# Optimization experiments

Hardware: AMD Instinct MI355X
Metric: run time of the kernel (lower is better)

The kernel has to match this reference:

```python
import jax, jax.numpy as jnp
import numpy as np

C = 512

def _xavier(key, shape, gain=1.0):
    fan_in, fan_out = shape[1], shape[0]
    a = gain * np.sqrt(6.0 / (fan_in + fan_out))
    return jax.random.uniform(key, shape, jnp.float32, -a, a)

def setup_inputs() -> dict:
    key = jax.random.key(0)
    ks = jax.random.split(key, 5)
    x = jax.random.normal(ks[0], (32, C, 32, 32), jnp.float32)
    # 1x1 conv weights as [out_ch, in_ch]; biases zero-init per module
    Wq = _xavier(ks[1], (C, C))
    Wk = _xavier(ks[2], (C, C))
    Wv = _xavier(ks[3], (C, C))
    Wo = _xavier(ks[4], (C, C), gain=1e-05)
    zeros = jnp.zeros((C,), jnp.float32)
    return {"x": x, "Wq": Wq, "bq": zeros, "Wk": Wk, "bk": zeros,
            "Wv": Wv, "bv": zeros, "Wo": Wo, "bo": zeros}

def _proj(x, W, b):
    # 1x1 conv: x [B,C,H,W], W [Cout,Cin] -> [B,Cout,H,W]
    return jnp.einsum('bchw,oc->bohw', x, W) + b[None, :, None, None]

def reference(x, Wq, bq, Wk, bk, Wv, bv, Wo, bo):
    B, Cc, H, W = x.shape
    q = _proj(x, Wq, bq).transpose(0, 2, 3, 1).reshape(B, H * W, Cc)  # [B,HW,C]
    k = _proj(x, Wk, bk).reshape(B, Cc, H * W)                        # [B,C,HW]
    v = _proj(x, Wv, bv).transpose(0, 2, 3, 1).reshape(B, H * W, Cc)  # [B,HW,C]
    w = jnp.einsum('bnc,bcm->bnm', q, k) * (Cc ** -0.5)               # [B,HW,HW]
    w = jax.nn.softmax(w, axis=-1)
    h = jnp.einsum('bnm,bmc->bnc', w, v)                              # [B,HW,C]
    h = h.reshape(B, H, W, Cc).transpose(0, 3, 1, 2)                  # [B,C,H,W]
    h = _proj(h, Wo, bo)
    return x + h
```

## Files before the change

### kernel.cpp

```cpp
#include <hip/hip_runtime.h>
#include <stdint.h>


#define CD 512
#define NSP 1024
#define SCALE_EXP2 0.06376339f

using bf16x8 = __attribute__((ext_vector_type(8))) short;
using f32x4  = __attribute__((ext_vector_type(4))) float;
typedef long i64v;

__device__ __forceinline__ unsigned short f2bf(float f) {
    union { float f; unsigned int i; } v; v.f = f;
    unsigned int r = v.i + 0x7FFFu + ((v.i >> 16) & 1u);
    return (unsigned short)(r >> 16);
}
__device__ __forceinline__ unsigned char f2f8(float f) {
    unsigned int r;
    asm("v_cvt_pk_fp8_f32 %0, %1, %1" : "=v"(r) : "v"(f));
    return (unsigned char)(r & 0xffu);
}
__device__ __forceinline__ unsigned int f4_to_f8x4(float a, float b, float c, float d) {
    unsigned int r = 0;
    asm("v_cvt_pk_fp8_f32 %0, %2, %3\n\t"
        "v_cvt_pk_fp8_f32 %0, %4, %5 op_sel:[0,0,1]"
        : "=v"(r) : "0"(r), "v"(a), "v"(b), "v"(c), "v"(d));
    return r;
}
__device__ __forceinline__ void gl_lds16(const void* g, void* l) {
    __builtin_amdgcn_global_load_lds(
        (const __attribute__((address_space(1))) void*)g,
        (__attribute__((address_space(3))) void*)l, 16, 0, 0);
}

__global__ __launch_bounds__(256) void cvt_all(
    const float* __restrict__ Wq, const float* __restrict__ Wk,
    const float* __restrict__ Wv, const float* __restrict__ Wo,
    const float* __restrict__ bq, const float* __restrict__ bk,
    unsigned char* __restrict__ w8, unsigned short* __restrict__ wob,
    float* __restrict__ bqk)
{
    int idx = blockIdx.x * 256 + threadIdx.x;
    int which = idx >> 18, off = idx & 262143;
    if (which < 3) {
        const float* src = which == 0 ? Wq : which == 1 ? Wk : Wv;
        w8[idx] = f2f8(src[off]);
    } else {
        wob[off] = f2bf(Wo[off]);
    }
    if (idx < 1024) bqk[idx] = (idx < 512) ? bq[idx] : bk[idx - 512];
}

__global__ __launch_bounds__(256) void transpose_x(const float* __restrict__ x,
                                                   unsigned char* __restrict__ xt) {
    __shared__ float t[32][33];
    int b = blockIdx.z;
    int n0 = blockIdx.x * 32, c0 = blockIdx.y * 32;
    const float* xb = x + (size_t)b * CD * NSP;
    unsigned char* xtb = xt + (size_t)b * NSP * CD;
    int tx = threadIdx.x, ty = threadIdx.y;
    #pragma unroll
    for (int i = 0; i < 4; ++i)
        t[ty + i * 8][tx] = xb[(size_t)(c0 + ty + i * 8) * NSP + n0 + tx];
    __syncthreads();
    #pragma unroll
    for (int i = 0; i < 4; ++i)
        xtb[(size_t)(n0 + ty + i * 8) * CD + c0 + tx] = f2f8(t[tx][ty + i * 8]);
}

template<int BIAS_MODE>
__global__ __launch_bounds__(256)
void gemm_bt8(const unsigned char* __restrict__ A,
              const unsigned char* __restrict__ B,
              unsigned char* __restrict__ C8,
              const float* __restrict__ bias,
              int K, int lda, int ldb, int ldc,
              long sA, long sB, long sC)
{
    __shared__ __align__(16) unsigned char As[2][128 * 64];
    __shared__ __align__(16) unsigned char Bs[2][128 * 64];

    const int z = blockIdx.z;
    const unsigned char* Ab = A + (size_t)z * sA + (size_t)blockIdx.y * 128 * lda;
    const unsigned char* Bb = B + (size_t)z * sB + (size_t)blockIdx.x * 128 * ldb;

    const int t = threadIdx.x;
    const int lane = t & 63;
    const int wave = t >> 6;
    const int wr = wave >> 1, wc = wave & 1;
    const int lr = lane & 15, lk = lane >> 4;

    f32x4 acc[4][4] = {};

    const int KT = K >> 6;
    auto stage = [&](int kt, int buf) {
        int k0 = kt << 6;
        #pragma unroll
        for (int i = 0; i < 2; ++i) {
            int rb = i * 64 + wave * 16;
            int row = rb + (lane >> 2);
            int src = (lane & 3) ^ ((row >> 1) & 3);
            gl_lds16(Ab + (size_t)row * lda + k0 + src * 16, &As[buf][rb * 64]);
            gl_lds16(Bb + (size_t)row * ldb + k0 + src * 16, &Bs[buf][rb * 64]);
        }
    };
    stage(0, 0);
    for (int kt = 0; kt < KT; ++kt) {
        int cur = kt & 1;
        if (kt + 1 < KT) {
            stage(kt + 1, cur ^ 1);
            asm volatile("s_waitcnt vmcnt(4)" ::: "memory");
        } else {
            asm volatile("s_waitcnt vmcnt(0)" ::: "memory");
        }
        __builtin_amdgcn_s_barrier();
        const unsigned char* Ac = &As[cur][0];
        const unsigned char* Bc = &Bs[cur][0];
        #pragma unroll
        for (int kk = 0; kk < 2; ++kk) {
            int c16 = kk * 2 + (lk >> 1);
            int half = (lk & 1) * 8;
            i64v af[4], bfr[4];
            #pragma unroll
            for (int f = 0; f < 4; ++f) {
                int arow = wr * 64 + f * 16 + lr;
                af[f] = *(const i64v*)&Ac[arow * 64 + ((c16 ^ ((arow >> 1) & 3)) << 4) + half];
                int brow = wc * 64 + f * 16 + lr;
                bfr[f] = *(const i64v*)&Bc[brow * 64 + ((c16 ^ ((brow >> 1) & 3)) << 4) + half];
            }
            #pragma unroll
            for (int fm = 0; fm < 4; ++fm)
                #pragma unroll
                for (int fn = 0; fn < 4; ++fn)
                    acc[fm][fn] = __builtin_amdgcn_mfma_f32_16x16x32_fp8_fp8(
                        af[fm], bfr[fn], acc[fm][fn], 0, 0, 0);
        }
        asm volatile("s_waitcnt lgkmcnt(0)" ::: "memory");
        __builtin_amdgcn_s_barrier();
    }

    const int m0 = blockIdx.y * 128;
    const int n0 = blockIdx.x * 128;
    unsigned char* Cp = C8 + (size_t)z * sC;
    #pragma unroll
    for (int fm = 0; fm < 4; ++fm) {
        #pragma unroll
        for (int fn = 0; fn < 4; ++fn) {
            int col = n0 + wc * 64 + fn * 16 + lr;
            int rowb = m0 + wr * 64 + fm * 16 + lk * 4;
            #pragma unroll
            for (int j = 0; j < 4; ++j) {
                int row = rowb + j;
                float v = acc[fm][fn][j];
                if (BIAS_MODE == 1) v += bias[col];
                if (BIAS_MODE == 2) v += bias[row];
                Cp[(size_t)row * ldc + col] = f2f8(v);
            }
        }
    }
}

__global__ __launch_bounds__(256)
void gemm_bt_out(const unsigned short* __restrict__ A,
                 const unsigned short* __restrict__ B,
                 float* __restrict__ Cf,
                 const float* __restrict__ bias,
                 const float* __restrict__ resid,
                 int K, int lda, int ldb, int ldc,
                 long sB, long sC, long sR)
{
    __shared__ __align__(16) unsigned short As[2][128 * 64];
    __shared__ __align__(16) unsigned short Bs[2][128 * 64];

    const int z = blockIdx.z;
    const unsigned short* Ab = A + (size_t)blockIdx.y * 128 * lda;
    const unsigned short* Bb = B + (size_t)z * sB + (size_t)blockIdx.x * 128 * ldb;

    const int t = threadIdx.x;
    const int lane = t & 63;
    const int wave = t >> 6;
    const int wr = wave >> 1, wc = wave & 1;
    const int lr = lane & 15, lk = lane >> 4;

    f32x4 acc[4][4] = {};

    const int KT = K >> 6;
    auto stage = [&](int kt, int buf) {
        int k0 = kt << 6;
        #pragma unroll
        for (int i = 0; i < 4; ++i) {
            int rb = i * 32 + wave * 8;
            int row = rb + (lane >> 3);
            int ch = (lane & 7) ^ (row & 7);
            gl_lds16(Ab + (size_t)row * lda + k0 + ch * 8, &As[buf][rb * 64]);
            gl_lds16(Bb + (size_t)row * ldb + k0 + ch * 8, &Bs[buf][rb * 64]);
        }
    };
    stage(0, 0);
    for (int kt = 0; kt < KT; ++kt) {
        int cur = kt & 1;
        if (kt + 1 < KT) {
            stage(kt + 1, cur ^ 1);
            asm volatile("s_waitcnt vmcnt(8)" ::: "memory");
        } else {
            asm volatile("s_waitcnt vmcnt(0)" ::: "memory");
        }
        __builtin_amdgcn_s_barrier();
        const unsigned short* Ac = &As[cur][0];
        const unsigned short* Bc = &Bs[cur][0];
        #pragma unroll
        for (int kk = 0; kk < 2; ++kk) {
            bf16x8 af[4], bfr[4];
            #pragma unroll
            for (int f = 0; f < 4; ++f) {
                int arow = wr * 64 + f * 16 + lr;
                af[f] = *(const bf16x8*)&Ac[(arow << 6) + ((((kk << 2) | lk) ^ (arow & 7)) << 3)];
                int brow = wc * 64 + f * 16 + lr;
                bfr[f] = *(const bf16x8*)&Bc[(brow << 6) + ((((kk << 2) | lk) ^ (brow & 7)) << 3)];
            }
            #pragma unroll
            for (int fm = 0; fm < 4; ++fm)
                #pragma unroll
                for (int fn = 0; fn < 4; ++fn)
                    acc[fm][fn] = __builtin_amdgcn_mfma_f32_16x16x32_bf16(
                        af[fm], bfr[fn], acc[fm][fn], 0, 0, 0);
        }
        asm volatile("s_waitcnt lgkmcnt(0)" ::: "memory");
        __builtin_amdgcn_s_barrier();
    }

    const int m0 = blockIdx.y * 128;
    const int n0 = blockIdx.x * 128;
    float* Co = Cf + (size_t)z * sC;
    const float* rp = resid + (size_t)z * sR;
    #pragma unroll
    for (int fm = 0; fm < 4; ++fm) {
        #pragma unroll
        for (int fn = 0; fn < 4; ++fn) {
            int col = n0 + wc * 64 + fn * 16 + lr;
            int rowb = m0 + wr * 64 + fm * 16 + lk * 4;
            #pragma unroll
            for (int j = 0; j < 4; ++j) {
                int row = rowb + j;
                float v = acc[fm][fn][j] + bias[row] + rp[(size_t)row * ldc + col];
                Co[(size_t)row * ldc + col] = v;
            }
        }
    }
}

__global__ __launch_bounds__(512, 2)
void flash_attn(const unsigned char* __restrict__ Q,
                const unsigned char* __restrict__ Kg,
                const unsigned char* __restrict__ Vg,
                unsigned short* __restrict__ H)
{
    __shared__ __align__(16) unsigned char Ks[2][64 * 512];
    __shared__ __align__(16) unsigned char Vs[2][512 * 64];
    __shared__ __align__(16) unsigned char Ps[128 * 72];
    __shared__ float Ls[128];
    __shared__ int flag;

    const int p = blockIdx.x;
    const int b  = ((p >> 6) << 3) + (p & 7);
    const int qt = (p >> 3) & 7;

    const int tid = threadIdx.x;
    const int w = tid >> 6, lane = tid & 63;
    const int lr = lane & 15, lk = lane >> 4;
    const int q0 = qt * 128 + w * 16;

    i64v qf[16];
    const unsigned char* qp = Q + ((size_t)b * NSP + q0 + lr) * 1024 + lk * 8;
    #pragma unroll
    for (int st = 0; st < 16; ++st) qf[st] = *(const i64v*)(qp + st * 32);

    f32x4 o[8][4] = {};
    float m = -3.0e38f, l = 0.f;

    const unsigned char* Kb = Kg + (size_t)b * NSP * 1024;
    const unsigned char* Vb = Vg + (size_t)b * CD * 1024;

    auto stageK = [&](int t, int buf) {
        int kv0 = t * 64;
        #pragma unroll
        for (int i = 0; i < 4; ++i) {
            int rb = i * 16 + w * 2;
            int row = rb + (lane >> 5);
            int src = (lane & 31) ^ (row & 7);
            gl_lds16(Kb + (size_t)(kv0 + row) * 1024 + src * 16, &Ks[buf][rb * 512]);
        }
    };
    auto stageV = [&](int t, int buf) {
        int kv0 = t * 64;
        #pragma unroll
        for (int i = 0; i < 4; ++i) {
            int cb = i * 128 + w * 16;
            int c = cb + (lane >> 2);
            int src = (lane & 3) ^ ((c >> 1) & 3);
            gl_lds16(Vb + (size_t)c * 1024 + kv0 + src * 16, &Vs[buf][cb * 64]);
        }
    };

    if (tid == 0) flag = -1;
    stageK(0, 0); stageV(0, 0);
    asm volatile("s_waitcnt vmcnt(0) lgkmcnt(0)" ::: "memory");
    __builtin_amdgcn_s_barrier();

    for (int t = 0; t < 16; ++t) {
        const int cur = t & 1;
        if (t < 15) { stageK(t + 1, cur ^ 1); stageV(t + 1, cur ^ 1); }

        f32x4 s[4] = {};
        const unsigned char* Kc = &Ks[cur][0];
        __builtin_amdgcn_s_setprio(1);
        #pragma unroll
        for (int st = 0; st < 16; ++st) {
            int c16 = st * 2 + (lk >> 1);
            int half = (lk & 1) * 8;
            #pragma unroll
            for (int kvf = 0; kvf < 4; ++kvf) {
                int row = kvf * 16 + lr;
                i64v kf = *(const i64v*)&Kc[row * 512 + ((c16 ^ (row & 7)) << 4) + half];
                s[kvf] = __builtin_amdgcn_mfma_f32_16x16x32_fp8_fp8(kf, qf[st], s[kvf], 0, 0, 0);
            }
        }
        __builtin_amdgcn_s_setprio(0);

        #pragma unroll
        for (int kvf = 0; kvf < 4; ++kvf)
            #pragma unroll
            for (int j = 0; j < 4; ++j) s[kvf][j] *= SCALE_EXP2;

        float pm = fmaxf(fmaxf(fmaxf(s[0][0], s[0][1]), fmaxf(s[0][2], s[0][3])),
                         fmaxf(fmaxf(s[1][0], s[1][1]), fmaxf(s[1][2], s[1][3])));
        pm = fmaxf(pm, fmaxf(fmaxf(fmaxf(s[2][0], s[2][1]), fmaxf(s[2][2], s[2][3])),
                             fmaxf(fmaxf(s[3][0], s[3][1]), fmaxf(s[3][2], s[3][3]))));
        pm = fmaxf(pm, __shfl_xor(pm, 16));
        pm = fmaxf(pm, __shfl_xor(pm, 32));
        bool ev = !__all(pm - m <= 8.0f);
        float mn = fmaxf(m, pm);
        float sc = ev ? exp2f(m - mn) : 1.0f;
        if (ev) { m = mn; l *= sc; }
        if (lk == 0) Ls[w * 16 + lr] = sc;
        if (ev && lane == 0) flag = t;

        float rs = 0.f;
        #pragma unroll
        for (int kvf = 0; kvf < 4; ++kvf)
            #pragma unroll
            for (int j = 0; j < 4; ++j) {
                s[kvf][j] = exp2f(s[kvf][j] - m);
                rs += s[kvf][j];
            }
        rs += __shfl_xor(rs, 16);
        rs += __shfl_xor(rs, 32);
        l += rs;

        #pragma unroll
        for (int kvf = 0; kvf < 4; ++kvf) {
            unsigned int pk = f4_to_f8x4(s[kvf][0], s[kvf][1], s[kvf][2], s[kvf][3]);
            *(unsigned int*)&Ps[(w * 16 + lr) * 72 + kvf * 16 + lk * 4] = pk;
        }
        asm volatile("s_waitcnt lgkmcnt(0)" ::: "memory");
        __builtin_amdgcn_s_barrier();

        if (flag == t) {
            #pragma unroll
            for (int qf2 = 0; qf2 < 8; ++qf2) {
                f32x4 scv = *(const f32x4*)&Ls[qf2 * 16 + lk * 4];
                #pragma unroll
                for (int cf = 0; cf < 4; ++cf) {
                    o[qf2][cf][0] *= scv[0]; o[qf2][cf][1] *= scv[1];
                    o[qf2][cf][2] *= scv[2]; o[qf2][cf][3] *= scv[3];
                }
            }
        }
        const unsigned char* Vc2 = &Vs[cur][0];
        __builtin_amdgcn_s_setprio(1);
        #pragma unroll
        for (int ks = 0; ks < 2; ++ks) {
            int c16 = ks * 2 + (lk >> 1);
            int half = (lk & 1) * 8;
            i64v vfr[4];
            #pragma unroll
            for (int cf = 0; cf < 4; ++cf) {
                int c = w * 64 + cf * 16 + lr;
                vfr[cf] = *(const i64v*)&Vc2[c * 64 + ((c16 ^ ((c >> 1) & 3)) << 4) + half];
            }
            #pragma unroll
            for (int qf2 = 0; qf2 < 8; ++qf2) {
                i64v pa = *(const i64v*)&Ps[(qf2 * 16 + lr) * 72 + ks * 32 + lk * 8];
                #pragma unroll
                for (int cf = 0; cf < 4; ++cf)
                    o[qf2][cf] = __builtin_amdgcn_mfma_f32_16x16x32_fp8_fp8(
                        pa, vfr[cf], o[qf2][cf], 0, 0, 0);
            }
        }
        __builtin_amdgcn_s_setprio(0);
        asm volatile("s_waitcnt vmcnt(0) lgkmcnt(0)" ::: "memory");
        __builtin_amdgcn_s_barrier();
    }

    if (lk == 0) Ls[w * 16 + lr] = 1.0f / l;
    asm volatile("s_waitcnt lgkmcnt(0)" ::: "memory");
    __builtin_amdgcn_s_barrier();
    unsigned short* Hp = H + ((size_t)b * NSP + qt * 128) * CD + w * 64;
    #pragma unroll
    for (int qf2 = 0; qf2 < 8; ++qf2) {
        f32x4 li = *(const f32x4*)&Ls[qf2 * 16 + lk * 4];
        #pragma unroll
        for (int cf = 0; cf < 4; ++cf) {
            #pragma unroll
            for (int j = 0; j < 4; ++j)
                Hp[(size_t)(qf2 * 16 + lk * 4 + j) * CD + cf * 16 + lr] = f2bf(o[qf2][cf][j] * li[j]);
        }
    }
}

extern "C" void kernel_launch(void* const* d_in, const int* in_sizes, int n_in,
                              void* d_out, int out_size, void* d_ws, size_t ws_size,
                              hipStream_t stream)
{
    const float* x  = (const float*)d_in[0];
    const float* Wq = (const float*)d_in[1];
    const float* bq = (const float*)d_in[2];
    const float* Wk = (const float*)d_in[3];
    const float* bk = (const float*)d_in[4];
    const float* Wv = (const float*)d_in[5];
    const float* bv = (const float*)d_in[6];
    const float* Wo = (const float*)d_in[7];
    const float* bo = (const float*)d_in[8];
    float* out = (float*)d_out;

    unsigned char* w = (unsigned char*)d_ws;
    unsigned char*  W8  = w;
    unsigned short* Wob = (unsigned short*)(w + 786432);
    float*          bqk = (float*)(w + 1310720);
    unsigned char*  Xt8 = w + 1314816;
    unsigned char*  QK8 = w + 18092032;
    unsigned char*  Vc8 = w + 51646464;
    unsigned short* Hb  = (unsigned short*)(w + 68423680);

    cvt_all<<<4096, 256, 0, stream>>>(Wq, Wk, Wv, Wo, bq, bk, W8, Wob, bqk);
    transpose_x<<<dim3(32, 16, 32), dim3(32, 8), 0, stream>>>(x, Xt8);

    gemm_bt8<1><<<dim3(8, 256, 1), 256, 0, stream>>>(
        Xt8, W8, QK8, bqk, 512, 512, 512, 1024, 0, 0, 0);

    gemm_bt8<2><<<dim3(8, 4, 32), 256, 0, stream>>>(
        W8 + 524288, Xt8, Vc8, bv, 512, 512, 512, 1024, 0, 524288, 524288);

    flash_attn<<<256, 512, 0, stream>>>(QK8, QK8 + 512, Vc8, Hb);

    gemm_bt_out<<<dim3(8, 4, 32), 256, 0, stream>>>(
        Wob, Hb, out, bo, x, 512, 512, 512, 1024, 524288, 524288, 524288);
}
```

Measured before the change: 205.0 us.

## Warp-specialize flash attention into QK-softmax and PV/loader wave groups

Splits the flash-attention block into 4 waves that compute QK scores and softmax (each handling 32 query rows) and 8 waves that stage K/V tiles and accumulate P·V. P, the rescale factors and the flags are double-buffered in LDS so that QK for tile t+1 overlaps PV for tile t, and staging runs two tiles ahead. The intent is to hide softmax and load latency behind the matrix units. In exchange the block grows to 768 threads with a tighter per-thread register budget, and correctness now depends on barrier counts matching exactly between the two wave groups.

```diff
diff --git a/kernel.cpp b/kernel.cpp
--- a/kernel.cpp
+++ b/kernel.cpp
@@ -249,7 +249,7 @@
     }
 }
 
-__global__ __launch_bounds__(512, 2)
+__global__ __launch_bounds__(768, 3)
 void flash_attn(const unsigned char* __restrict__ Q,
                 const unsigned char* __restrict__ Kg,
                 const unsigned char* __restrict__ Vg,
@@ -257,9 +257,10 @@
 {
     __shared__ __align__(16) unsigned char Ks[2][64 * 512];
     __shared__ __align__(16) unsigned char Vs[2][512 * 64];
-    __shared__ __align__(16) unsigned char Ps[128 * 72];
-    __shared__ float Ls[128];
-    __shared__ int flag;
+    __shared__ __align__(16) unsigned char Ps[2][128 * 72];
+    __shared__ __align__(16) float Ls[2][128];
+    __shared__ __align__(16) float Lfin[128];
+    __shared__ int flags[2];
 
     const int p = blockIdx.x;
     const int b  = ((p >> 6) << 3) + (p & 7);
@@ -268,152 +269,185 @@
     const int tid = threadIdx.x;
     const int w = tid >> 6, lane = tid & 63;
     const int lr = lane & 15, lk = lane >> 4;
-    const int q0 = qt * 128 + w * 16;
-
-    i64v qf[16];
-    const unsigned char* qp = Q + ((size_t)b * NSP + q0 + lr) * 1024 + lk * 8;
-    #pragma unroll
-    for (int st = 0; st < 16; ++st) qf[st] = *(const i64v*)(qp + st * 32);
-
-    f32x4 o[8][4] = {};
-    float m = -3.0e38f, l = 0.f;
+
+    if (tid == 0) { flags[0] = -1; flags[1] = -1; }
 
     const unsigned char* Kb = Kg + (size_t)b * NSP * 1024;
     const unsigned char* Vb = Vg + (size_t)b * CD * 1024;
 
-    auto stageK = [&](int t, int buf) {
-        int kv0 = t * 64;
-        #pragma unroll
-        for (int i = 0; i < 4; ++i) {
-            int rb = i * 16 + w * 2;
-            int row = rb + (lane >> 5);
-            int src = (lane & 31) ^ (row & 7);
-            gl_lds16(Kb + (size_t)(kv0 + row) * 1024 + src * 16, &Ks[buf][rb * 512]);
-        }
-    };
-    auto stageV = [&](int t, int buf) {
-        int kv0 = t * 64;
-        #pragma unroll
-        for (int i = 0; i < 4; ++i) {
-            int cb = i * 128 + w * 16;
-            int c = cb + (lane >> 2);
-            int src = (lane & 3) ^ ((c >> 1) & 3);
-            gl_lds16(Vb + (size_t)c * 1024 + kv0 + src * 16, &Vs[buf][cb * 64]);
-        }
-    };
-
-    if (tid == 0) flag = -1;
-    stageK(0, 0); stageV(0, 0);
-    asm volatile("s_waitcnt vmcnt(0) lgkmcnt(0)" ::: "memory");
-    __builtin_amdgcn_s_barrier();
-
-    for (int t = 0; t < 16; ++t) {
-        const int cur = t & 1;
-        if (t < 15) { stageK(t + 1, cur ^ 1); stageV(t + 1, cur ^ 1); }
-
-        f32x4 s[4] = {};
-        const unsigned char* Kc = &Ks[cur][0];
-        __builtin_amdgcn_s_setprio(1);
+    if (w < 4) {
+        const int q0 = qt * 128 + w * 32;
+        i64v qf0[16], qf1[16];
+        const unsigned char* qp = Q + ((size_t)b * NSP + q0 + lr) * 1024 + lk * 8;
         #pragma unroll
         for (int st = 0; st < 16; ++st) {
-            int c16 = st * 2 + (lk >> 1);
-            int half = (lk & 1) * 8;
+            qf0[st] = *(const i64v*)(qp + st * 32);
+            qf1[st] = *(const i64v*)(qp + 16 * 1024 + st * 32);
+        }
+        float m0 = -3.0e38f, m1 = -3.0e38f, l0 = 0.f, l1 = 0.f;
+
+        auto qksm = [&](int tau) {
+            const int pb = tau & 1;
+            const unsigned char* Kc = &Ks[pb][0];
+            f32x4 s0[4] = {}, s1[4] = {};
+            __builtin_amdgcn_s_setprio(1);
+            #pragma unroll
+            for (int st = 0; st < 16; ++st) {
+                int c16 = st * 2 + (lk >> 1);
+                int half = (lk & 1) * 8;
+                #pragma unroll
+                for (int kvf = 0; kvf < 4; ++kvf) {
+                    int row = kvf * 16 + lr;
+                    i64v kf = *(const i64v*)&Kc[row * 512 + ((c16 ^ (row & 7)) << 4) + half];
+                    s0[kvf] = __builtin_amdgcn_mfma_f32_16x16x32_fp8_fp8(kf, qf0[st], s0[kvf], 0, 0, 0);
+                    s1[kvf] = __builtin_amdgcn_mfma_f32_16x16x32_fp8_fp8(kf, qf1[st], s1[kvf], 0, 0, 0);
+                }
+            }
+            __builtin_amdgcn_s_setprio(0);
+            #pragma unroll
+            for (int kvf = 0; kvf < 4; ++kvf)
+                #pragma unroll
+                for (int j = 0; j < 4; ++j) {
+                    s0[kvf][j] *= SCALE_EXP2;
+                    s1[kvf][j] *= SCALE_EXP2;
+                }
+            float pm0 = fmaxf(fmaxf(fmaxf(s0[0][0], s0[0][1]), fmaxf(s0[0][2], s0[0][3])),
+                              fmaxf(fmaxf(s0[1][0], s0[1][1]), fmaxf(s0[1][2], s0[1][3])));
+            pm0 = fmaxf(pm0, fmaxf(fmaxf(fmaxf(s0[2][0], s0[2][1]), fmaxf(s0[2][2], s0[2][3])),
+                                   fmaxf(fmaxf(s0[3][0], s0[3][1]), fmaxf(s0[3][2], s0[3][3]))));
+            float pm1 = fmaxf(fmaxf(fmaxf(s1[0][0], s1[0][1]), fmaxf(s1[0][2], s1[0][3])),
+                              fmaxf(fmaxf(s1[1][0], s1[1][1]), fmaxf(s1[1][2], s1[1][3])));
+            pm1 = fmaxf(pm1, fmaxf(fmaxf(fmaxf(s1[2][0], s1[2][1]), fmaxf(s1[2][2], s1[2][3])),
+                                   fmaxf(fmaxf(s1[3][0], s1[3][1]), fmaxf(s1[3][2], s1[3][3]))));
+            pm0 = fmaxf(pm0, __shfl_xor(pm0, 16));
+            pm0 = fmaxf(pm0, __shfl_xor(pm0, 32));
+            pm1 = fmaxf(pm1, __shfl_xor(pm1, 16));
+            pm1 = fmaxf(pm1, __shfl_xor(pm1, 32));
+            bool ev = !__all(fmaxf(pm0 - m0, pm1 - m1) <= 8.0f);
+            float sc0 = 1.f, sc1 = 1.f;
+            if (ev) {
+                float n0 = fmaxf(m0, pm0); sc0 = exp2f(m0 - n0); m0 = n0; l0 *= sc0;
+                float n1 = fmaxf(m1, pm1); sc1 = exp2f(m1 - n1); m1 = n1; l1 *= sc1;
+            }
+            if (lk == 0) { Ls[pb][w * 32 + lr] = sc0; Ls[pb][w * 32 + 16 + lr] = sc1; }
+            if (ev && lane == 0) flags[pb] = tau;
+            float rs0 = 0.f, rs1 = 0.f;
             #pragma unroll
             for (int kvf = 0; kvf < 4; ++kvf) {
-                int row = kvf * 16 + lr;
-                i64v kf = *(const i64v*)&Kc[row * 512 + ((c16 ^ (row & 7)) << 4) + half];
-                s[kvf] = __builtin_amdgcn_mfma_f32_16x16x32_fp8_fp8(kf, qf[st], s[kvf], 0, 0, 0);
-            }
-        }
-        __builtin_amdgcn_s_setprio(0);
-
-        #pragma unroll
-        for (int kvf = 0; kvf < 4; ++kvf)
-            #pragma unroll
-            for (int j = 0; j < 4; ++j) s[kvf][j] *= SCALE_EXP2;
-
-        float pm = fmaxf(fmaxf(fmaxf(s[0][0], s[0][1]), fmaxf(s[0][2], s[0][3])),
-                         fmaxf(fmaxf(s[1][0], s[1][1]), fmaxf(s[1][2], s[1][3])));
-        pm = fmaxf(pm, fmaxf(fmaxf(fmaxf(s[2][0], s[2][1]), fmaxf(s[2][2], s[2][3])),
-                             fmaxf(fmaxf(s[3][0], s[3][1]), fmaxf(s[3][2], s[3][3]))));
-        pm = fmaxf(pm, __shfl_xor(pm, 16));
-        pm = fmaxf(pm, __shfl_xor(pm, 32));
-        bool ev = !__all(pm - m <= 8.0f);
-        float mn = fmaxf(m, pm);
-        float sc = ev ? exp2f(m - mn) : 1.0f;
-        if (ev) { m = mn; l *= sc; }
-        if (lk == 0) Ls[w * 16 + lr] = sc;
-        if (ev && lane == 0) flag = t;
-
-        float rs = 0.f;
-        #pragma unroll
-        for (int kvf = 0; kvf < 4; ++kvf)
-            #pragma unroll
-            for (int j = 0; j < 4; ++j) {
-                s[kvf][j] = exp2f(s[kvf][j] - m);
-                rs += s[kvf][j];
-            }
-        rs += __shfl_xor(rs, 16);
-        rs += __shfl_xor(rs, 32);
-        l += rs;
-
-        #pragma unroll
-        for (int kvf = 0; kvf < 4; ++kvf) {
-            unsigned int pk = f4_to_f8x4(s[kvf][0], s[kvf][1], s[kvf][2], s[kvf][3]);
-            *(unsigned int*)&Ps[(w * 16 + lr) * 72 + kvf * 16 + lk * 4] = pk;
-        }
+                #pragma unroll
+                for (int j = 0; j < 4; ++j) {
+                    s0[kvf][j] = exp2f(s0[kvf][j] - m0); rs0 += s0[kvf][j];
+                    s1[kvf][j] = exp2f(s1[kvf][j] - m1); rs1 += s1[kvf][j];
+                }
+                unsigned int pk0 = f4_to_f8x4(s0[kvf][0], s0[kvf][1], s0[kvf][2], s0[kvf][3]);
+                unsigned int pk1 = f4_to_f8x4(s1[kvf][0], s1[kvf][1], s1[kvf][2], s1[kvf][3]);
+                *(unsigned int*)&Ps[pb][(w * 32 + lr) * 72 + kvf * 16 + lk * 4] = pk0;
+                *(unsigned int*)&Ps[pb][(w * 32 + 16 + lr) * 72 + kvf * 16 + lk * 4] = pk1;
+            }
+            rs0 += __shfl_xor(rs0, 16); rs0 += __shfl_xor(rs0, 32); l0 += rs0;
+            rs1 += __shfl_xor(rs1, 16); rs1 += __shfl_xor(rs1, 32); l1 += rs1;
+        };
+
+        __builtin_amdgcn_s_barrier();
+        qksm(0);
         asm volatile("s_waitcnt lgkmcnt(0)" ::: "memory");
         __builtin_amdgcn_s_barrier();
-
-        if (flag == t) {
-            #pragma unroll
-            for (int qf2 = 0; qf2 < 8; ++qf2) {
-                f32x4 scv = *(const f32x4*)&Ls[qf2 * 16 + lk * 4];
+        for (int t = 0; t < 16; ++t) {
+            if (t < 15) qksm(t + 1);
+            asm volatile("s_waitcnt lgkmcnt(0)" ::: "memory");
+            __builtin_amdgcn_s_barrier();
+        }
+        if (lk == 0) { Lfin[w * 32 + lr] = 1.f / l0; Lfin[w * 32 + 16 + lr] = 1.f / l1; }
+        asm volatile("s_waitcnt lgkmcnt(0)" ::: "memory");
+        __builtin_amdgcn_s_barrier();
+    } else {
+        const int wp = w - 4;
+        auto stageK = [&](int t, int buf) {
+            int kv0 = t * 64;
+            #pragma unroll
+            for (int i = 0; i < 4; ++i) {
+                int rb = i * 16 + wp * 2;
+                int row = rb + (lane >> 5);
+                int src = (lane & 31) ^ (row & 7);
+                gl_lds16(Kb + (size_t)(kv0 + row) * 1024 + src * 16, &Ks[buf][rb * 512]);
+            }
+        };
+        auto stageV = [&](int t, int buf) {
+            int kv0 = t * 64;
+            #pragma unroll
+            for (int i = 0; i < 4; ++i) {
+                int cb = wp * 64 + i * 16;
+                int c = cb + (lane >> 2);
+                int src = (lane & 3) ^ ((c >> 1) & 3);
+                gl_lds16(Vb + (size_t)c * 1024 + kv0 + src * 16, &Vs[buf][cb * 64]);
+            }
+        };
+        f32x4 o[8][4] = {};
+
+        stageK(0, 0); stageV(0, 0);
+        asm volatile("s_waitcnt vmcnt(0)" ::: "memory");
+        __builtin_amdgcn_s_barrier();
+        stageK(1, 1); stageV(1, 1);
+        asm volatile("s_waitcnt vmcnt(0)" ::: "memory");
+        __builtin_amdgcn_s_barrier();
+
+        for (int t = 0; t < 16; ++t) {
+            const int pb = t & 1;
+            if (t < 14) stageK(t + 2, pb);
+            if (flags[pb] == t) {
+                #pragma unroll
+                for (int qf2 = 0; qf2 < 8; ++qf2) {
+                    f32x4 scv = *(const f32x4*)&Ls[pb][qf2 * 16 + lk * 4];
+                    #pragma unroll
+                    for (int cf = 0; cf < 4; ++cf) {
+                        o[qf2][cf][0] *= scv[0]; o[qf2][cf][1] *= scv[1];
+                        o[qf2][cf][2] *= scv[2]; o[qf2][cf][3] *= scv[3];
+                    }
+                }
+            }
+            const unsigned char* Vc = &Vs[pb][0];
+            __builtin_amdgcn_s_setprio(1);
+            #pragma unroll
+            for (int ks = 0; ks < 2; ++ks) {
+                int c16 = ks * 2 + (lk >> 1);
+                int half = (lk & 1) * 8;
+                i64v vfr[4];
                 #pragma unroll
                 for (int cf = 0; cf < 4; ++cf) {
-                    o[qf2][cf][0] *= scv[0]; o[qf2][cf][1] *= scv[1];
-                    o[qf2][cf][2] *= scv[2]; o[qf2][cf][3] *= scv[3];
-                }
-            }
-        }
-        const unsigned char* Vc2 = &Vs[cur][0];
-        __builtin_amdgcn_s_setprio(1);
-        #pragma unroll
-        for (int ks = 0; ks < 2; ++ks) {
-            int c16 = ks * 2 + (lk >> 1);
-            int half = (lk & 1) * 8;
-            i64v vfr[4];
+                    int c = wp * 64 + cf * 16 + lr;
+                    vfr[cf] = *(const i64v*)&Vc[c * 64 + ((c16 ^ ((c >> 1) & 3)) << 4) + half];
+                }
+                #pragma unroll
+                for (int qf2 = 0; qf2 < 8; ++qf2) {
+                    i64v pa = *(const i64v*)&Ps[pb][(qf2 * 16 + lr) * 72 + ks * 32 + lk * 8];
+                    #pragma unroll
+                    for (int cf = 0; cf < 4; ++cf)
+                        o[qf2][cf] = __builtin_amdgcn_mfma_f32_16x16x32_fp8_fp8(
+                            pa, vfr[cf], o[qf2][cf], 0, 0, 0);
+                }
+            }
+            __builtin_amdgcn_s_setprio(0);
+            asm volatile("s_waitcnt lgkmcnt(0)" ::: "memory");
+            if (t < 14) {
+                stageV(t + 2, pb);
+                asm volatile("s_waitcnt vmcnt(4)" ::: "memory");
+            } else {
+                asm volatile("s_waitcnt vmcnt(0)" ::: "memory");
+            }
+            __builtin_amdgcn_s_barrier();
+        }
+        __builtin_amdgcn_s_barrier();
+        unsigned short* Hp = H + ((size_t)b * NSP + qt * 128) * CD + wp * 64;
+        #pragma unroll
+        for (int qf2 = 0; qf2 < 8; ++qf2) {
+            f32x4 li = *(const f32x4*)&Lfin[qf2 * 16 + lk * 4];
             #pragma unroll
             for (int cf = 0; cf < 4; ++cf) {
-                int c = w * 64 + cf * 16 + lr;
-                vfr[cf] = *(const i64v*)&Vc2[c * 64 + ((c16 ^ ((c >> 1) & 3)) << 4) + half];
-            }
-            #pragma unroll
-            for (int qf2 = 0; qf2 < 8; ++qf2) {
-                i64v pa = *(const i64v*)&Ps[(qf2 * 16 + lr) * 72 + ks * 32 + lk * 8];
-                #pragma unroll
-                for (int cf = 0; cf < 4; ++cf)
-                    o[qf2][cf] = __builtin_amdgcn_mfma_f32_16x16x32_fp8_fp8(
-                        pa, vfr[cf], o[qf2][cf], 0, 0, 0);
-            }
-        }
-        __builtin_amdgcn_s_setprio(0);
-        asm volatile("s_waitcnt vmcnt(0) lgkmcnt(0)" ::: "memory");
-        __builtin_amdgcn_s_barrier();
-    }
-
-    if (lk == 0) Ls[w * 16 + lr] = 1.0f / l;
-    asm volatile("s_waitcnt lgkmcnt(0)" ::: "memory");
-    __builtin_amdgcn_s_barrier();
-    unsigned short* Hp = H + ((size_t)b * NSP + qt * 128) * CD + w * 64;
-    #pragma unroll
-    for (int qf2 = 0; qf2 < 8; ++qf2) {
-        f32x4 li = *(const f32x4*)&Ls[qf2 * 16 + lk * 4];
-        #pragma unroll
-        for (int cf = 0; cf < 4; ++cf) {
-            #pragma unroll
-            for (int j = 0; j < 4; ++j)
-                Hp[(size_t)(qf2 * 16 + lk * 4 + j) * CD + cf * 16 + lr] = f2bf(o[qf2][cf][j] * li[j]);
+                #pragma unroll
+                for (int j = 0; j < 4; ++j)
+                    Hp[(size_t)(qf2 * 16 + lk * 4 + j) * CD + cf * 16 + lr] =
+                        f2bf(o[qf2][cf][j] * li[j]);
+            }
         }
     }
 }
@@ -451,7 +485,7 @@
     gemm_bt8<2><<<dim3(8, 4, 32), 256, 0, stream>>>(
         W8 + 524288, Xt8, Vc8, bv, 512, 512, 512, 1024, 0, 524288, 524288);
 
-    flash_attn<<<256, 512, 0, stream>>>(QK8, QK8 + 512, Vc8, Hb);
+    flash_attn<<<256, 768, 0, stream>>>(QK8, QK8 + 512, Vc8, Hb);
 
     gemm_bt_out<<<dim3(8, 4, 32), 256, 0, stream>>>(
         Wob, Hb, out, bo, x, 512, 512, 512, 1024, 524288, 524288, 524288);
```

Result: slower. 212.8 us (+3.8%).
